# Kernel optimization log

Hardware: AMD Instinct MI355X
Metric: run time of the kernel (lower is better)

## Reference

```python
import jax, jax.numpy as jnp
import numpy as np

S, T, B, E, H, V = 64, 64, 64, 256, 256, 32000
PAD = 0


def _lstm_layer(X, Wih, Whh, b, h0, c0):
    # X: (time, B, in), torch gate order i,f,g,o
    def step(carry, x_t):
        h, c = carry
        z = x_t @ Wih.T + h @ Whh.T + b
        i, f, g, o = jnp.split(z, 4, axis=-1)
        c = jax.nn.sigmoid(f) * c + jax.nn.sigmoid(i) * jnp.tanh(g)
        h = jax.nn.sigmoid(o) * jnp.tanh(c)
        return (h, c), h
    (hT, cT), outs = jax.lax.scan(step, (h0, c0), X)
    return outs, hT, cT


def setup_inputs() -> dict:
    key = jax.random.key(0)
    ks = jax.random.split(key, 20)
    p = lambda k, shape: (jax.random.normal(k, shape, jnp.float32) * 0.05)
    inp = {
        "source_padded": jax.random.randint(ks[0], (S, B), 0, V, jnp.int32),
        "target_padded": jax.random.randint(ks[1], (T, B), 0, V, jnp.int32),
        "src_emb": p(ks[2], (V, E)),
        "tgt_emb": p(ks[3], (V, E)),
        "enc_Wih_f": p(ks[4], (4 * H, E)),
        "enc_Whh_f": p(ks[5], (4 * H, H)),
        "enc_b_f": p(ks[6], (4 * H,)),
        "enc_Wih_b": p(ks[7], (4 * H, E)),
        "enc_Whh_b": p(ks[8], (4 * H, H)),
        "enc_b_b": p(ks[9], (4 * H,)),
        "dec_Wih": p(ks[10], (4 * H, E + H)),
        "dec_Whh": p(ks[11], (4 * H, H)),
        "dec_b": p(ks[12], (4 * H,)),
        "Wh": p(ks[13], (H, 2 * H)),
        "Wc": p(ks[14], (H, 2 * H)),
        "Watt": p(ks[15], (H, 2 * H)),
        "Wcomb": p(ks[16], (H, 3 * H)),
        "Wvocab": p(ks[17], (V, H)),
    }
    return inp


def reference(source_padded, target_padded, src_emb, tgt_emb,
              enc_Wih_f, enc_Whh_f, enc_b_f, enc_Wih_b, enc_Whh_b, enc_b_b,
              dec_Wih, dec_Whh, dec_b, Wh, Wc, Watt, Wcomb, Wvocab):
    X = src_emb[source_padded]                      # (S,B,E)
    h0 = jnp.zeros((B, H), X.dtype)
    c0 = jnp.zeros((B, H), X.dtype)
    # bidirectional encoder (all sequences full length -> pack is identity)
    fwd_out, hf, cf = _lstm_layer(X, enc_Wih_f, enc_Whh_f, enc_b_f, h0, c0)
    bwd_out, hb, cb = _lstm_layer(X[::-1], enc_Wih_b, enc_Whh_b, enc_b_b, h0, c0)
    bwd_out = bwd_out[::-1]
    enc_hiddens = jnp.concatenate([fwd_out, bwd_out], -1).transpose(1, 0, 2)  # (B,S,2H)
    dec_h = jnp.concatenate([hf, hb], -1) @ Wh.T     # h_projection
    dec_c = jnp.concatenate([cf, cb], -1) @ Wc.T     # c_projection
    enc_proj = enc_hiddens @ Watt.T                  # (B,S,H)

    Y = tgt_emb[target_padded[:-1]]                  # (T-1,B,E)

    def dstep(carry, Y_t):
        h, c, o_prev = carry
        x = jnp.concatenate([Y_t, o_prev], -1)       # (B,E+H)
        z = x @ dec_Wih.T + h @ dec_Whh.T + dec_b
        i, f, g, o = jnp.split(z, 4, axis=-1)
        c = jax.nn.sigmoid(f) * c + jax.nn.sigmoid(i) * jnp.tanh(g)
        h = jax.nn.sigmoid(o) * jnp.tanh(c)
        e_t = jnp.einsum('bsh,bh->bs', enc_proj, h)  # attention scores
        alpha = jax.nn.softmax(e_t, axis=-1)         # no pads -> mask is no-op
        a_t = jnp.einsum('bs,bsd->bd', alpha, enc_hiddens)  # context (B,2H)
        O_t = jnp.tanh(jnp.concatenate([a_t, h], -1) @ Wcomb.T)  # dropout=eval
        return (h, c, O_t), O_t

    _, outs = jax.lax.scan(dstep, (dec_h, dec_c, jnp.zeros((B, H), X.dtype)), Y)
    P = jax.nn.log_softmax(outs @ Wvocab.T, axis=-1)          # (T-1,B,V)
    gold = jnp.take_along_axis(P, target_padded[1:][..., None], axis=-1)[..., 0]
    tmask = (target_padded[1:] != PAD).astype(P.dtype)
    return (gold * tmask).sum(axis=0)                          # (B,)
```

## Files before the change

kernel.cpp:

```cpp
#include <hip/hip_runtime.h>
#include <hip/hip_bf16.h>

static constexpr int S = 64, T = 64, B = 64, E = 256, H = 256, V = 32000;
static constexpr int H4 = 4 * H;
static constexpr int NCHUNK = 500;
static constexpr int NROW = (T - 1) * B;
static constexpr int LDP = 264;

typedef short bf16x8 __attribute__((ext_vector_type(8)));
typedef float f32x4 __attribute__((ext_vector_type(4)));
typedef unsigned long long ull;

__device__ __forceinline__ float sigf(float x) { return 1.0f / (1.0f + __expf(-x)); }
__device__ __forceinline__ float tanhfast(float x) { return 1.0f - 2.0f / (__expf(2.0f * x) + 1.0f); }
__device__ __forceinline__ float bflo(uint w) { return __uint_as_float(w << 16); }
__device__ __forceinline__ float bfhi(uint w) { return __uint_as_float(w & 0xffff0000u); }
__device__ __forceinline__ ushort f2bu(float x) {
  return __bfloat16_as_ushort(__float2bfloat16(x));
}

__device__ __forceinline__ void st_u32(uint* p, uint v) {
  __hip_atomic_store(p, v, __ATOMIC_RELAXED, __HIP_MEMORY_SCOPE_AGENT);
}
__device__ __forceinline__ uint ld_u32(const uint* p) {
  return __hip_atomic_load(p, __ATOMIC_RELAXED, __HIP_MEMORY_SCOPE_AGENT);
}
__device__ __forceinline__ void st_u64(ull* p, ull v) {
  __hip_atomic_store(p, v, __ATOMIC_RELAXED, __HIP_MEMORY_SCOPE_AGENT);
}
__device__ __forceinline__ ull ld_u64(const ull* p) {
  return __hip_atomic_load(p, __ATOMIC_RELAXED, __HIP_MEMORY_SCOPE_AGENT);
}
__device__ __forceinline__ ull pack2f(float a, float b) {
  return ((ull)__float_as_uint(b) << 32) | (ull)__float_as_uint(a);
}

__global__ __launch_bounds__(256) void k_cvt_bf16(const float* __restrict__ src,
                                                  __hip_bfloat16* __restrict__ dst, int n) {
  int i = blockIdx.x * 256 + threadIdx.x;
  if (i < n) dst[i] = __float2bfloat16(src[i]);
}

__global__ __launch_bounds__(256) void k_cvt_slice(const float* __restrict__ src,
                                                   __hip_bfloat16* __restrict__ dst) {
  int n = blockIdx.x, tid = threadIdx.x;
  dst[n * 256 + tid] = __float2bfloat16(src[n * 512 + tid]);
}

__global__ __launch_bounds__(256) void k_gather(const int* __restrict__ idx,
                                                const float* __restrict__ emb,
                                                __hip_bfloat16* __restrict__ dst) {
  int r = blockIdx.x, tid = threadIdx.x;
  dst[r * 256 + tid] = __float2bfloat16(emb[idx[r] * E + tid]);
}

__global__ __launch_bounds__(256) void k_pack4(const float* __restrict__ src,
                                               uint2* __restrict__ dst,
                                               int total, int jshift, int ld, int off) {
  int idx = blockIdx.x * 256 + threadIdx.x;
  if (idx >= total) return;
  int J = 1 << jshift;
  int i = idx >> jshift, j = idx & (J - 1);
  const float* s = src + (size_t)j * ld + off + 4 * i;
  float4 v = *(const float4*)s;
  uint2 o;
  o.x = (uint)f2bu(v.x) | ((uint)f2bu(v.y) << 16);
  o.y = (uint)f2bu(v.z) | ((uint)f2bu(v.w) << 16);
  dst[(size_t)i * J + j] = o;
}

__global__ __launch_bounds__(256) void k_xdec_init(const float* __restrict__ dech0,
                                                   __hip_bfloat16* __restrict__ Xd) {
  int b = blockIdx.x, tid = threadIdx.x;
  Xd[b * 512 + tid] = __float2bfloat16(dech0[b * 256 + tid]);
  Xd[b * 512 + 256 + tid] = __float2bfloat16(0.f);
}

#define MFMA_TILE_BODY(Abase, Wbase, rb, cb)                                     \
  const int tid = threadIdx.x;                                                   \
  const int lane = tid & 63, wid = tid >> 6;                                     \
  const int wr = wid >> 1, wc = wid & 1;                                         \
  const int l15 = lane & 15, l4 = lane >> 4;                                     \
  for (int it = 0; it < 8; it++) {                                               \
    int c = it * 256 + tid;                                                      \
    int row = c >> 5, off = (c & 31) * 8;                                        \
    *(uint4*)&Asl[row * LDP + off] =                                             \
        *(const uint4*)((Abase) + (size_t)((rb) + row) * 256 + off);             \
    *(uint4*)&Bsl[row * LDP + off] =                                             \
        *(const uint4*)((Wbase) + (size_t)((cb) + row) * 256 + off);             \
  }                                                                              \
  __syncthreads();                                                               \
  f32x4 acc[2][2];                                                               \
  for (int m = 0; m < 2; m++)                                                    \
    for (int n = 0; n < 2; n++) acc[m][n] = (f32x4){0.f, 0.f, 0.f, 0.f};         \
  for (int kk = 0; kk < 8; kk++) {                                               \
    int ko = kk * 32 + l4 * 8;                                                   \
    bf16x8 a0 = *(const bf16x8*)&Asl[(wr * 32 + l15) * LDP + ko];                \
    bf16x8 a1 = *(const bf16x8*)&Asl[(wr * 32 + 16 + l15) * LDP + ko];           \
    bf16x8 b0 = *(const bf16x8*)&Bsl[(wc * 32 + l15) * LDP + ko];                \
    bf16x8 b1 = *(const bf16x8*)&Bsl[(wc * 32 + 16 + l15) * LDP + ko];           \
    acc[0][0] = __builtin_amdgcn_mfma_f32_16x16x32_bf16(a0, b0, acc[0][0], 0, 0, 0); \
    acc[0][1] = __builtin_amdgcn_mfma_f32_16x16x32_bf16(a0, b1, acc[0][1], 0, 0, 0); \
    acc[1][0] = __builtin_amdgcn_mfma_f32_16x16x32_bf16(a1, b0, acc[1][0], 0, 0, 0); \
    acc[1][1] = __builtin_amdgcn_mfma_f32_16x16x32_bf16(a1, b1, acc[1][1], 0, 0, 0); \
  }

__global__ __launch_bounds__(256) void k_gemm_bias(
    const __hip_bfloat16* __restrict__ A, const __hip_bfloat16* __restrict__ W,
    const float* __restrict__ bias, float* __restrict__ C, int ldc) {
  __shared__ __align__(16) ushort Asl[64 * LDP];
  __shared__ __align__(16) ushort Bsl[64 * LDP];
  const int cb = blockIdx.x * 64, rb = blockIdx.y * 64;
  MFMA_TILE_BODY((const ushort*)A, (const ushort*)W, rb, cb)
  #pragma unroll
  for (int m = 0; m < 2; m++)
    #pragma unroll
    for (int n = 0; n < 2; n++) {
      int col = cb + wc * 32 + n * 16 + l15;
      float bv = bias[col];
      #pragma unroll
      for (int r = 0; r < 4; r++) {
        int row = rb + wr * 32 + m * 16 + l4 * 4 + r;
        C[(size_t)row * ldc + col] = acc[m][n][r] + bv;
      }
    }
}

__global__ __launch_bounds__(256) void k_encproj_mfma(
    const __hip_bfloat16* __restrict__ fwd_bf, const __hip_bfloat16* __restrict__ bwd_bf,
    const __hip_bfloat16* __restrict__ Watt_bf, __hip_bfloat16* __restrict__ encproj_bf) {
  __shared__ __align__(16) ushort Asl[64 * LDP];
  __shared__ __align__(16) ushort Bsl[64 * LDP];
  const int cb = blockIdx.x * 64, rb = blockIdx.y * 64;
  const int tid = threadIdx.x;
  const int lane = tid & 63, wid = tid >> 6;
  const int wr = wid >> 1, wc = wid & 1;
  const int l15 = lane & 15, l4 = lane >> 4;
  f32x4 acc[2][2];
  #pragma unroll
  for (int m = 0; m < 2; m++)
    #pragma unroll
    for (int n = 0; n < 2; n++) acc[m][n] = (f32x4){0.f, 0.f, 0.f, 0.f};
  for (int kt = 0; kt < 2; kt++) {
    if (kt) __syncthreads();
    for (int it = 0; it < 8; it++) {
      int c = it * 256 + tid;
      int row = c >> 5, off = (c & 31) * 8;
      int r = rb + row, s = r >> 6, bb = r & 63;
      const ushort* arow = (kt == 0)
          ? (const ushort*)fwd_bf + (size_t)(s * 64 + bb) * 256
          : (const ushort*)bwd_bf + (size_t)(s * 64 + bb) * 256;
      *(uint4*)&Asl[row * LDP + off] = *(const uint4*)(arow + off);
      *(uint4*)&Bsl[row * LDP + off] =
          *(const uint4*)((const ushort*)Watt_bf + (size_t)(cb + row) * 512 + kt * 256 + off);
    }
    __syncthreads();
    for (int kk = 0; kk < 8; kk++) {
      int ko = kk * 32 + l4 * 8;
      bf16x8 a0 = *(const bf16x8*)&Asl[(wr * 32 + l15) * LDP + ko];
      bf16x8 a1 = *(const bf16x8*)&Asl[(wr * 32 + 16 + l15) * LDP + ko];
      bf16x8 b0 = *(const bf16x8*)&Bsl[(wc * 32 + l15) * LDP + ko];
      bf16x8 b1 = *(const bf16x8*)&Bsl[(wc * 32 + 16 + l15) * LDP + ko];
      acc[0][0] = __builtin_amdgcn_mfma_f32_16x16x32_bf16(a0, b0, acc[0][0], 0, 0, 0);
      acc[0][1] = __builtin_amdgcn_mfma_f32_16x16x32_bf16(a0, b1, acc[0][1], 0, 0, 0);
      acc[1][0] = __builtin_amdgcn_mfma_f32_16x16x32_bf16(a1, b0, acc[1][0], 0, 0, 0);
      acc[1][1] = __builtin_amdgcn_mfma_f32_16x16x32_bf16(a1, b1, acc[1][1], 0, 0, 0);
    }
  }
  #pragma unroll
  for (int m = 0; m < 2; m++)
    #pragma unroll
    for (int n = 0; n < 2; n++) {
      int col = cb + wc * 32 + n * 16 + l15;
      #pragma unroll
      for (int r = 0; r < 4; r++) {
        int row = rb + wr * 32 + m * 16 + l4 * 4 + r;
        int s = row >> 6, bb = row & 63;
        ((ushort*)encproj_bf)[(size_t)(bb * 64 + s) * 256 + col] = f2bu(acc[m][n][r]);
      }
    }
}

__global__ __launch_bounds__(256) void k_vocab2(
    const __hip_bfloat16* __restrict__ outs_bf, const __hip_bfloat16* __restrict__ Wv,
    const int* __restrict__ tgt, float* __restrict__ part_max,
    float* __restrict__ part_sum, float* __restrict__ gold) {
  __shared__ __align__(16) ushort Asl[64 * LDP];
  __shared__ __align__(16) ushort Bsl[64 * LDP];
  __shared__ int goldcol[64];
  __shared__ float pm[64][2], ps[64][2];
  const int vb = blockIdx.x;
  const int tid = threadIdx.x;
  const int lane = tid & 63, wid = tid >> 6;
  const int wr = wid >> 1, wc = wid & 1;
  const int l15 = lane & 15, l4 = lane >> 4;
  for (int it = 0; it < 8; it++) {
    int c = it * 256 + tid;
    int row = c >> 5, off = (c & 31) * 8;
    *(uint4*)&Bsl[row * LDP + off] =
        *(const uint4*)((const ushort*)Wv + (size_t)(vb * 64 + row) * 256 + off);
  }
  for (int t = 0; t < T - 1; t++) {
    __syncthreads();
    for (int it = 0; it < 8; it++) {
      int c = it * 256 + tid;
      int row = c >> 5, off = (c & 31) * 8;
      *(uint4*)&Asl[row * LDP + off] =
          *(const uint4*)((const ushort*)outs_bf + (size_t)(t * 64 + row) * 256 + off);
    }
    if (tid < 64) goldcol[tid] = tgt[(t + 1) * B + tid];
    __syncthreads();
    f32x4 acc[2][2];
    #pragma unroll
    for (int m = 0; m < 2; m++)
      #pragma unroll
      for (int n = 0; n < 2; n++) acc[m][n] = (f32x4){0.f, 0.f, 0.f, 0.f};
    for (int kk = 0; kk < 8; kk++) {
      int ko = kk * 32 + l4 * 8;
      bf16x8 a0 = *(const bf16x8*)&Asl[(wr * 32 + l15) * LDP + ko];
      bf16x8 a1 = *(const bf16x8*)&Asl[(wr * 32 + 16 + l15) * LDP + ko];
      bf16x8 b0 = *(const bf16x8*)&Bsl[(wc * 32 + l15) * LDP + ko];
      bf16x8 b1 = *(const bf16x8*)&Bsl[(wc * 32 + 16 + l15) * LDP + ko];
      acc[0][0] = __builtin_amdgcn_mfma_f32_16x16x32_bf16(a0, b0, acc[0][0], 0, 0, 0);
      acc[0][1] = __builtin_amdgcn_mfma_f32_16x16x32_bf16(a0, b1, acc[0][1], 0, 0, 0);
      acc[1][0] = __builtin_amdgcn_mfma_f32_16x16x32_bf16(a1, b0, acc[1][0], 0, 0, 0);
      acc[1][1] = __builtin_amdgcn_mfma_f32_16x16x32_bf16(a1, b1, acc[1][1], 0, 0, 0);
    }
    #pragma unroll
    for (int m = 0; m < 2; m++) {
      #pragma unroll
      for (int r = 0; r < 4; r++) {
        int row_local = wr * 32 + m * 16 + l4 * 4 + r;
        int gc = goldcol[row_local];
        #pragma unroll
        for (int n = 0; n < 2; n++) {
          int col = vb * 64 + wc * 32 + n * 16 + l15;
          if (col == gc) gold[t * 64 + row_local] = acc[m][n][r];
        }
        float v = fmaxf(acc[m][0][r], acc[m][1][r]);
        #pragma unroll
        for (int o = 1; o < 16; o <<= 1) v = fmaxf(v, __shfl_xor(v, o));
        float e = __expf(acc[m][0][r] - v) + __expf(acc[m][1][r] - v);
        #pragma unroll
        for (int o = 1; o < 16; o <<= 1) e += __shfl_xor(e, o);
        if (l15 == 0) { pm[row_local][wc] = v; ps[row_local][wc] = e; }
      }
    }
    __syncthreads();
    if (tid < 64) {
      float m0 = pm[tid][0], m1 = pm[tid][1];
      float M = fmaxf(m0, m1);
      float Ss = ps[tid][0] * __expf(m0 - M) + ps[tid][1] * __expf(m1 - M);
      part_max[(size_t)vb * NROW + t * 64 + tid] = M;
      part_sum[(size_t)vb * NROW + t * 64 + tid] = Ss;
    }
  }
}

__global__ __launch_bounds__(256) void k_enc4(
    const float* __restrict__ XwF, const float* __restrict__ XwB,
    const float* __restrict__ WhhF, const float* __restrict__ WhhB,
    uint* __restrict__ Xenc_u32,
    __hip_bfloat16* __restrict__ fwd_bf, __hip_bfloat16* __restrict__ bwd_bf,
    float* __restrict__ Cfin, uint* __restrict__ eflags) {
  __shared__ __align__(16) ushort Wl[128 * 264];
  __shared__ __align__(16) ushort Xa[16 * 264];
  __shared__ float zz[4][8][33];
  __shared__ float hsb[8][32];
  const int id = blockIdx.x;
  const int g = id & 7, kb = id >> 3;
  const int dir = kb >> 3, s = kb & 7;
  const int tid = threadIdx.x;
  const float* Whh = dir ? WhhB : WhhF;
  const float* Xw = dir ? XwB : XwF;
  uint* fl = eflags + (size_t)(g * 2 + dir) * 8 * 32;
  for (int i = tid; i < 128 * 256; i += 256) {
    int c = i >> 8, k2 = i & 255;
    int gate = c >> 5, jj = c & 31;
    Wl[c * 264 + k2] = f2bu(Whh[(size_t)(gate * 256 + s * 32 + jj) * 256 + k2]);
  }
  for (int i = tid; i < 16 * 264; i += 256) Xa[i] = 0;
  const int lane = tid & 63, w = tid >> 6;
  const int l15 = lane & 15, l4 = lane >> 4;
  const int tb = tid >> 5, tjj = tid & 31;
  float c_reg = 0.f;
  __syncthreads();
  for (int st = 0; st < 64; st++) {
    const int ts = dir ? 63 - st : st;
    const int par = st & 1;
    const uint* Xr = Xenc_u32 + (size_t)(par * 2 + dir) * 8192;
    uint* Xo = Xenc_u32 + (size_t)((par ^ 1) * 2 + dir) * 8192;
    for (int i = tid; i < 8 * 128; i += 256) {
      int row = i >> 7, colu = i & 127;
      uint v = ld_u32(Xr + (size_t)(8 * g + row) * 128 + colu);
      *(uint*)&Xa[row * 264 + colu * 2] = v;
    }
    __syncthreads();
    f32x4 a0v = (f32x4){0.f, 0.f, 0.f, 0.f}, a1v = (f32x4){0.f, 0.f, 0.f, 0.f};
    for (int kk = 0; kk < 8; kk++) {
      bf16x8 af = *(const bf16x8*)&Xa[l15 * 264 + kk * 32 + l4 * 8];
      bf16x8 b0 = *(const bf16x8*)&Wl[((2 * w) * 16 + l15) * 264 + kk * 32 + l4 * 8];
      bf16x8 b1 = *(const bf16x8*)&Wl[((2 * w + 1) * 16 + l15) * 264 + kk * 32 + l4 * 8];
      a0v = __builtin_amdgcn_mfma_f32_16x16x32_bf16(af, b0, a0v, 0, 0, 0);
      a1v = __builtin_amdgcn_mfma_f32_16x16x32_bf16(af, b1, a1v, 0, 0, 0);
    }
    if (l4 < 2) {
      #pragma unroll
      for (int r = 0; r < 4; r++) {
        int b = l4 * 4 + r;
        zz[w][b][l15] = a0v[r];
        zz[w][b][16 + l15] = a1v[r];
      }
    }
    __syncthreads();
    {
      int gb = 8 * g + tb, j = 32 * s + tjj;
      const float* xw = Xw + (size_t)(ts * 64 + gb) * 1024;
      float zi = zz[0][tb][tjj] + xw[j];
      float zf = zz[1][tb][tjj] + xw[256 + j];
      float zg = zz[2][tb][tjj] + xw[512 + j];
      float zo = zz[3][tb][tjj] + xw[768 + j];
      float c = sigf(zf) * c_reg + sigf(zi) * tanhfast(zg);
      c_reg = c;
      float h = sigf(zo) * tanhfast(c);
      hsb[tb][tjj] = h;
      ushort hb = f2bu(h);
      if (dir == 0) ((ushort*)fwd_bf)[(size_t)(st * 64 + gb) * 256 + j] = hb;
      else          ((ushort*)bwd_bf)[(size_t)((63 - st) * 64 + gb) * 256 + j] = hb;
    }
    __syncthreads();
    if (tid < 128) {
      int tb2 = tid >> 4, p = tid & 15;
      uint v = (uint)f2bu(hsb[tb2][2 * p]) | ((uint)f2bu(hsb[tb2][2 * p + 1]) << 16);
      st_u32(Xo + (size_t)(8 * g + tb2) * 128 + 16 * s + p, v);
    }
    __syncthreads();
    if (tid == 0) st_u32(&fl[s * 32], (uint)(st + 1));
    if (tid < 8)
      while (ld_u32(&fl[tid * 32]) < (uint)(st + 1)) __builtin_amdgcn_s_sleep(2);
    asm volatile("" ::: "memory");
    __syncthreads();
  }
  Cfin[(size_t)(dir * 64 + 8 * g + tb) * 256 + 32 * s + tjj] = c_reg;
}

__global__ __launch_bounds__(256) void k_dec_init2(
    const __hip_bfloat16* __restrict__ Xenc, const float* __restrict__ Cfin,
    const float* __restrict__ Wh, const float* __restrict__ Wc,
    float* __restrict__ dech0, float* __restrict__ decc0) {
  int b = blockIdx.x, tid = threadIdx.x;
  __shared__ __align__(16) float ch[512], cc[512];
  ch[tid]       = __bfloat162float(Xenc[(size_t)(0 * 64 + b) * 256 + tid]);
  ch[256 + tid] = __bfloat162float(Xenc[(size_t)(1 * 64 + b) * 256 + tid]);
  cc[tid]       = Cfin[(size_t)(0 * 64 + b) * 256 + tid];
  cc[256 + tid] = Cfin[(size_t)(1 * 64 + b) * 256 + tid];
  __syncthreads();
  const float* wh = Wh + tid * 512;
  const float* wc = Wc + tid * 512;
  float ah = 0, ac = 0;
  for (int k = 0; k < 512; k += 4) {
    float4 hv = *(const float4*)&ch[k];
    float4 cv = *(const float4*)&cc[k];
    float4 w1 = *(const float4*)&wh[k];
    float4 w2 = *(const float4*)&wc[k];
    ah += hv.x * w1.x + hv.y * w1.y + hv.z * w1.z + hv.w * w1.w;
    ac += cv.x * w2.x + cv.y * w2.y + cv.z * w2.z + cv.w * w2.w;
  }
  dech0[b * 256 + tid] = ah;
  decc0[b * 256 + tid] = ac;
}

__global__ __launch_bounds__(512) void k_dec4(
    const float* __restrict__ YW, const float* __restrict__ dWih,
    const float* __restrict__ dWhh, const uint2* __restrict__ Wcq,
    const __hip_bfloat16* __restrict__ encproj_bf,
    const __hip_bfloat16* __restrict__ fwd_bf, const __hip_bfloat16* __restrict__ bwd_bf,
    const float* __restrict__ decc0, uint* __restrict__ Xd_u32,
    ull* __restrict__ zbuf_u64, __hip_bfloat16* __restrict__ outs_bf,
    uint* __restrict__ zflags, uint* __restrict__ aflags) {
  __shared__ __align__(16) char smem[153856];
  const int id = blockIdx.x;
  const int g = id & 7, kb = id >> 3;
  const int tid = threadIdx.x;
  uint* zfl = zflags + (size_t)g * 8 * 32;
  uint* afl = aflags + (size_t)g * 16 * 32;

  if (kb < 8) {
    const int s = kb;
    ushort* Wl = (ushort*)smem;
    ushort* Xa = (ushort*)(smem + 133120);
    float* zslds = (float*)(smem + 149760);
    for (int i = tid; i < 128 * 512; i += 512) {
      int c = i >> 9, k2 = i & 511;
      int gr = 128 * s + c;
      float v = (k2 < 256) ? dWhh[(size_t)gr * 256 + k2]
                           : dWih[(size_t)gr * 512 + 256 + (k2 - 256)];
      Wl[c * 520 + k2] = f2bu(v);
    }
    for (int i = tid; i < 16 * 520; i += 512) Xa[i] = 0;
    const int lane = tid & 63, w = tid >> 6;
    const int l15 = lane & 15, l4 = lane >> 4;
    __syncthreads();
    for (int t = 0; t < 63; t++) {
      if (t > 0) {
        if (tid < 16)
          while (ld_u32(&afl[tid * 32]) < (uint)t) __builtin_amdgcn_s_sleep(2);
        asm volatile("" ::: "memory");
        __syncthreads();
      }
      const uint* Xr = Xd_u32 + (size_t)(t & 1) * 16384;
      for (int i = tid; i < 8 * 256; i += 512) {
        int row = i >> 8, colu = i & 255;
        uint v = ld_u32(Xr + (size_t)(8 * g + row) * 256 + colu);
        *(uint*)&Xa[row * 520 + colu * 2] = v;
      }
      __syncthreads();
      f32x4 accv = (f32x4){0.f, 0.f, 0.f, 0.f};
      for (int kk = 0; kk < 16; kk++) {
        bf16x8 af = *(const bf16x8*)&Xa[l15 * 520 + kk * 32 + l4 * 8];
        bf16x8 bf = *(const bf16x8*)&Wl[(w * 16 + l15) * 520 + kk * 32 + l4 * 8];
        accv = __builtin_amdgcn_mfma_f32_16x16x32_bf16(af, bf, accv, 0, 0, 0);
      }
      if (l4 < 2) {
        #pragma unroll
        for (int r = 0; r < 4; r++) {
          int b = l4 * 4 + r;
          zslds[b * 128 + w * 16 + l15] = accv[r];
        }
      }
      __syncthreads();
      {
        int b = tid >> 6, cp = tid & 63;
        ull v = pack2f(zslds[b * 128 + 2 * cp], zslds[b * 128 + 2 * cp + 1]);
        st_u64(zbuf_u64 + (size_t)(8 * g + b) * 512 + 64 * s + cp, v);
      }
      __syncthreads();
      if (tid == 0) st_u32(&zfl[s * 32], (uint)(t + 1));
    }
  } else {
    const int lb = (kb - 8) >> 1, jh = (kb - 8) & 1;
    const int b = 8 * g + lb;
    ushort* ep = (ushort*)smem;
    ushort* eh = (ushort*)(smem + 33792);
    float* hn = (float*)(smem + 100352);
    float* xcomb = (float*)(smem + 101376);
    float* e_l = (float*)(smem + 104448);
    float* alpha_l = (float*)(smem + 104704);
    float* op_l = (float*)(smem + 104960);
    float* zstage = (float*)(smem + 107008);
    float* Ost = (float*)(smem + 111104);
    for (int i = tid; i < 64 * 256; i += 512) {
      int s2 = i >> 8, k2 = i & 255;
      ep[s2 * 264 + k2] = ((const ushort*)encproj_bf)[(size_t)(b * 64 + s2) * 256 + k2];
    }
    for (int i = tid; i < 64 * 512; i += 512) {
      int s2 = i >> 9, d = i & 511;
      ushort v = (d < 256) ? ((const ushort*)fwd_bf)[(size_t)(s2 * 64 + b) * 256 + d]
                           : ((const ushort*)bwd_bf)[(size_t)(s2 * 64 + b) * 256 + d - 256];
      eh[s2 * 520 + d] = v;
    }
    float c_reg = (tid < 256) ? decc0[(size_t)b * 256 + tid] : 0.f;
    __syncthreads();
    for (int t = 0; t < 63; t++) {
      if (tid < 8)
        while (ld_u32(&zfl[tid * 32]) < (uint)(t + 1)) __builtin_amdgcn_s_sleep(2);
      asm volatile("" ::: "memory");
      __syncthreads();
      {
        ull v = ld_u64(zbuf_u64 + (size_t)b * 512 + tid);
        ((ull*)zstage)[tid] = v;
      }
      __syncthreads();
      if (tid < 256) {
        const float* yw = YW + (size_t)(t * 64 + b) * 1024;
        float zi = zstage[tid] + yw[tid];
        float zf = zstage[256 + tid] + yw[256 + tid];
        float zg = zstage[512 + tid] + yw[512 + tid];
        float zo = zstage[768 + tid] + yw[768 + tid];
        float c = sigf(zf) * c_reg + sigf(zi) * tanhfast(zg);
        c_reg = c;
        hn[tid] = sigf(zo) * tanhfast(c);
      }
      __syncthreads();
      if (jh == 0 && tid < 128) {
        uint v = (uint)f2bu(hn[2 * tid]) | ((uint)f2bu(hn[2 * tid + 1]) << 16);
        st_u32(Xd_u32 + (size_t)((t & 1) ^ 1) * 16384 + (size_t)b * 256 + tid, v);
      }
      {
        int s2 = tid >> 3, q8 = tid & 7;
        const ushort* pr = ep + s2 * 264 + q8 * 32;
        const float* hq = hn + q8 * 32;
        float a = 0.f;
        #pragma unroll 8
        for (int kk = 0; kk < 32; kk += 2) {
          uint wv = *(const uint*)(pr + kk);
          a += bflo(wv) * hq[kk] + bfhi(wv) * hq[kk + 1];
        }
        a += __shfl_xor(a, 1);
        a += __shfl_xor(a, 2);
        a += __shfl_xor(a, 4);
        if (q8 == 0) e_l[s2] = a;
      }
      __syncthreads();
      if (tid < 64) {
        float e = e_l[tid];
        float mx = e;
        #pragma unroll
        for (int o = 32; o > 0; o >>= 1) mx = fmaxf(mx, __shfl_xor(mx, o));
        float p = __expf(e - mx);
        float ss = p;
        #pragma unroll
        for (int o = 32; o > 0; o >>= 1) ss += __shfl_xor(ss, o);
        alpha_l[tid] = p / ss;
      }
      __syncthreads();
      {
        float a = 0.f;
        const ushort* col = eh + tid;
        #pragma unroll 8
        for (int s2 = 0; s2 < 64; s2++)
          a += alpha_l[s2] * __uint_as_float(((uint)col[s2 * 520]) << 16);
        xcomb[tid] = a;
        if (tid < 256) xcomb[512 + tid] = hn[tid];
      }
      __syncthreads();
      {
        int jl = tid & 127, kq = tid >> 7;
        int j = jh * 128 + jl;
        const uint2* wp = Wcq + (size_t)(kq * 48) * 256 + j;
        const float4* x4 = (const float4*)xcomb + kq * 48;
        float a = 0.f;
        #pragma unroll 6
        for (int ii = 0; ii < 48; ii++) {
          uint2 wv = wp[(size_t)ii * 256];
          float4 xv = x4[ii];
          a += bflo(wv.x) * xv.x + bfhi(wv.x) * xv.y + bflo(wv.y) * xv.z + bfhi(wv.y) * xv.w;
        }
        op_l[kq * 128 + jl] = a;
      }
      __syncthreads();
      if (tid < 128) {
        float sum = op_l[tid] + op_l[128 + tid] + op_l[256 + tid] + op_l[384 + tid];
        float O = tanhfast(sum);
        Ost[tid] = O;
        ((ushort*)outs_bf)[(size_t)(t * 64 + b) * 256 + jh * 128 + tid] = f2bu(O);
      }
      __syncthreads();
      if (tid < 64) {
        uint v = (uint)f2bu(Ost[2 * tid]) | ((uint)f2bu(Ost[2 * tid + 1]) << 16);
        st_u32(Xd_u32 + (size_t)((t & 1) ^ 1) * 16384 + (size_t)b * 256 + 128 + jh * 64 + tid, v);
      }
      __syncthreads();
      if (tid == 0) st_u32(&afl[(lb * 2 + jh) * 32], (uint)(t + 1));
    }
  }
}

__global__ __launch_bounds__(256) void k_final(
    const float* __restrict__ part_max, const float* __restrict__ part_sum,
    const float* __restrict__ gold, const int* __restrict__ tgt,
    float* __restrict__ out) {
  int b = blockIdx.x, tid = threadIdx.x;
  int tq = tid >> 2, q = tid & 3;
  __shared__ float lm[64][4], ls[64][4];
  __shared__ float red[64];
  if (tq < T - 1) {
    int n = tq * B + b;
    float m = -__builtin_inff(), s = 0;
    for (int i = q; i < NCHUNK; i += 4) {
      float pmv = part_max[(size_t)i * NROW + n];
      float psv = part_sum[(size_t)i * NROW + n];
      float M2 = fmaxf(m, pmv);
      s = s * __expf(m - M2) + psv * __expf(pmv - M2);
      m = M2;
    }
    lm[tq][q] = m;
    ls[tq][q] = s;
  }
  __syncthreads();
  if (tid < T - 1) {
    float M = fmaxf(fmaxf(lm[tid][0], lm[tid][1]), fmaxf(lm[tid][2], lm[tid][3]));
    float Ss = ls[tid][0] * __expf(lm[tid][0] - M) + ls[tid][1] * __expf(lm[tid][1] - M) +
               ls[tid][2] * __expf(lm[tid][2] - M) + ls[tid][3] * __expf(lm[tid][3] - M);
    float lse = M + logf(Ss);
    int g = tgt[(tid + 1) * B + b];
    red[tid] = (g != 0) ? (gold[tid * B + b] - lse) : 0.f;
  }
  if (tid == T - 1) red[T - 1] = 0.f;
  __syncthreads();
  if (tid == 0) {
    float s = 0;
    for (int i = 0; i < T - 1; i++) s += red[i];
    out[b] = s;
  }
}

extern "C" void kernel_launch(void* const* d_in, const int* in_sizes, int n_in,
                              void* d_out, int out_size, void* d_ws, size_t ws_size,
                              hipStream_t stream) {
  (void)in_sizes; (void)n_in; (void)out_size; (void)ws_size;
  const int*   src   = (const int*)  d_in[0];
  const int*   tgt   = (const int*)  d_in[1];
  const float* semb  = (const float*)d_in[2];
  const float* temb  = (const float*)d_in[3];
  const float* WihF  = (const float*)d_in[4];
  const float* WhhF  = (const float*)d_in[5];
  const float* bF    = (const float*)d_in[6];
  const float* WihB  = (const float*)d_in[7];
  const float* WhhB  = (const float*)d_in[8];
  const float* bB    = (const float*)d_in[9];
  const float* dWih  = (const float*)d_in[10];
  const float* dWhh  = (const float*)d_in[11];
  const float* db    = (const float*)d_in[12];
  const float* Wh    = (const float*)d_in[13];
  const float* Wc    = (const float*)d_in[14];
  const float* Watt  = (const float*)d_in[15];
  const float* Wcomb = (const float*)d_in[16];
  const float* Wv    = (const float*)d_in[17];
  float* out = (float*)d_out;

  char* wp = (char*)d_ws;
  auto alloc = [&](size_t bytes) -> char* {
    char* p = wp;
    wp += (bytes + 255) & ~(size_t)255;
    return p;
  };
  float* XwF  = (float*)alloc((size_t)S * B * H4 * 4);
  float* XwB  = (float*)alloc((size_t)S * B * H4 * 4);
  float* YW   = (float*)alloc((size_t)(T - 1) * B * H4 * 4);
  __hip_bfloat16* fwd_bf     = (__hip_bfloat16*)alloc((size_t)S * B * H * 2);
  __hip_bfloat16* bwd_bf     = (__hip_bfloat16*)alloc((size_t)S * B * H * 2);
  __hip_bfloat16* encproj_bf = (__hip_bfloat16*)alloc((size_t)B * S * H * 2);
  __hip_bfloat16* Ag         = (__hip_bfloat16*)alloc((size_t)S * B * E * 2);
  __hip_bfloat16* Yg         = (__hip_bfloat16*)alloc((size_t)(T - 1) * B * E * 2);
  __hip_bfloat16* WihF_bf    = (__hip_bfloat16*)alloc((size_t)H4 * E * 2);
  __hip_bfloat16* WihB_bf    = (__hip_bfloat16*)alloc((size_t)H4 * E * 2);
  __hip_bfloat16* dWih_bf    = (__hip_bfloat16*)alloc((size_t)H4 * E * 2);
  __hip_bfloat16* Wv_bf      = (__hip_bfloat16*)alloc((size_t)V * H * 2);
  __hip_bfloat16* Watt_bf    = (__hip_bfloat16*)alloc((size_t)H * 512 * 2);
  __hip_bfloat16* outs_bf    = (__hip_bfloat16*)alloc((size_t)NROW * H * 2);
  uint2* Wcq = (uint2*)alloc((size_t)192 * 256 * 8);
  float* part_max = (float*)alloc((size_t)NCHUNK * NROW * 4);
  float* part_sum = (float*)alloc((size_t)NCHUNK * NROW * 4);
  float* gold     = (float*)alloc((size_t)NROW * 4);
  float* Cfin  = (float*)alloc((size_t)2 * B * H * 4);
  float* dech0 = (float*)alloc((size_t)B * H * 4);
  float* decc0 = (float*)alloc((size_t)B * H * 4);
  ull* zbuf_u64 = (ull*)alloc((size_t)B * 512 * 8);
  __hip_bfloat16* Xenc = (__hip_bfloat16*)alloc((size_t)2 * 2 * B * H * 2);
  __hip_bfloat16* Xdec = (__hip_bfloat16*)alloc((size_t)2 * B * 512 * 2);
  char* stateBase = wp;
  uint* eflags = (uint*)alloc(16 * 8 * 32 * 4);
  uint* zflags = (uint*)alloc(8 * 8 * 32 * 4);
  uint* aflags = (uint*)alloc(8 * 16 * 32 * 4);
  size_t stateBytes = (size_t)(wp - stateBase);
  hipMemsetAsync(stateBase, 0, stateBytes, stream);
  hipMemsetAsync(Xenc, 0, (size_t)2 * 2 * B * H * 2, stream);

  hipLaunchKernelGGL(k_cvt_bf16, dim3((H4 * E + 255) / 256), dim3(256), 0, stream,
                     WihF, WihF_bf, H4 * E);
  hipLaunchKernelGGL(k_cvt_bf16, dim3((H4 * E + 255) / 256), dim3(256), 0, stream,
                     WihB, WihB_bf, H4 * E);
  hipLaunchKernelGGL(k_cvt_slice, dim3(H4), dim3(256), 0, stream, dWih, dWih_bf);
  hipLaunchKernelGGL(k_cvt_bf16, dim3((V * H + 255) / 256), dim3(256), 0, stream,
                     Wv, Wv_bf, V * H);
  hipLaunchKernelGGL(k_cvt_bf16, dim3((H * 512 + 255) / 256), dim3(256), 0, stream,
                     Watt, Watt_bf, H * 512);
  hipLaunchKernelGGL(k_gather, dim3(S * B), dim3(256), 0, stream, src, semb, Ag);
  hipLaunchKernelGGL(k_gather, dim3((T - 1) * B), dim3(256), 0, stream, tgt, temb, Yg);
  hipLaunchKernelGGL(k_pack4, dim3(192 * 256 / 256), dim3(256), 0, stream,
                     Wcomb, Wcq, 192 * 256, 8, 768, 0);

  hipLaunchKernelGGL(k_gemm_bias, dim3(H4 / 64, S * B / 64), dim3(256), 0, stream,
                     Ag, WihF_bf, bF, XwF, H4);
  hipLaunchKernelGGL(k_gemm_bias, dim3(H4 / 64, S * B / 64), dim3(256), 0, stream,
                     Ag, WihB_bf, bB, XwB, H4);
  hipLaunchKernelGGL(k_gemm_bias, dim3(H4 / 64, (T - 1) * B / 64), dim3(256), 0, stream,
                     Yg, dWih_bf, db, YW, H4);

  hipLaunchKernelGGL(k_enc4, dim3(128), dim3(256), 0, stream,
                     XwF, XwB, WhhF, WhhB, (uint*)Xenc, fwd_bf, bwd_bf, Cfin, eflags);
  hipLaunchKernelGGL(k_dec_init2, dim3(B), dim3(256), 0, stream,
                     Xenc, Cfin, Wh, Wc, dech0, decc0);
  hipLaunchKernelGGL(k_xdec_init, dim3(B), dim3(256), 0, stream, dech0, Xdec);
  hipLaunchKernelGGL(k_encproj_mfma, dim3(4, 64), dim3(256), 0, stream,
                     fwd_bf, bwd_bf, Watt_bf, encproj_bf);

  hipLaunchKernelGGL(k_dec4, dim3(192), dim3(512), 0, stream,
                     YW, dWih, dWhh, Wcq, encproj_bf, fwd_bf, bwd_bf,
                     decc0, (uint*)Xdec, zbuf_u64, outs_bf, zflags, aflags);

  hipLaunchKernelGGL(k_vocab2, dim3(NCHUNK), dim3(256), 0, stream,
                     outs_bf, Wv_bf, tgt, part_max, part_sum, gold);
  hipLaunchKernelGGL(k_final, dim3(B), dim3(256), 0, stream,
                     part_max, part_sum, gold, tgt, out);
}
```

Baseline: 1.251 ms.

## Move decoder LSTM cell update into gate-GEMM blocks, drop z exchange buffer

The decoder gate-GEMM blocks now own complete i/f/g/o rows for their 32 hidden units. They apply the LSTM cell nonlinearity locally, keeping c in a register, and write bf16 h straight into the double-buffered Xdec. The attention blocks no longer read a fp32 z buffer or compute the cell; they just load h. This removes one global round trip of 64x1024 floats per step from the serial critical path. Separately, dec_init and xdec_init are fused into one kernel. In exchange, GEMM blocks must also wait on zflags from peer GEMM blocks to avoid overwriting Xdec early.

```diff
diff --git a/kernel.cpp b/kernel.cpp
--- a/kernel.cpp
+++ b/kernel.cpp
@@ -24,15 +24,6 @@
 }
 __device__ __forceinline__ uint ld_u32(const uint* p) {
   return __hip_atomic_load(p, __ATOMIC_RELAXED, __HIP_MEMORY_SCOPE_AGENT);
-}
-__device__ __forceinline__ void st_u64(ull* p, ull v) {
-  __hip_atomic_store(p, v, __ATOMIC_RELAXED, __HIP_MEMORY_SCOPE_AGENT);
-}
-__device__ __forceinline__ ull ld_u64(const ull* p) {
-  return __hip_atomic_load(p, __ATOMIC_RELAXED, __HIP_MEMORY_SCOPE_AGENT);
-}
-__device__ __forceinline__ ull pack2f(float a, float b) {
-  return ((ull)__float_as_uint(b) << 32) | (ull)__float_as_uint(a);
 }
 
 __global__ __launch_bounds__(256) void k_cvt_bf16(const float* __restrict__ src,
@@ -67,13 +58,6 @@
   o.x = (uint)f2bu(v.x) | ((uint)f2bu(v.y) << 16);
   o.y = (uint)f2bu(v.z) | ((uint)f2bu(v.w) << 16);
   dst[(size_t)i * J + j] = o;
-}
-
-__global__ __launch_bounds__(256) void k_xdec_init(const float* __restrict__ dech0,
-                                                   __hip_bfloat16* __restrict__ Xd) {
-  int b = blockIdx.x, tid = threadIdx.x;
-  Xd[b * 512 + tid] = __float2bfloat16(dech0[b * 256 + tid]);
-  Xd[b * 512 + 256 + tid] = __float2bfloat16(0.f);
 }
 
 #define MFMA_TILE_BODY(Abase, Wbase, rb, cb)                                     \
@@ -344,12 +328,13 @@
   Cfin[(size_t)(dir * 64 + 8 * g + tb) * 256 + 32 * s + tjj] = c_reg;
 }
 
-__global__ __launch_bounds__(256) void k_dec_init2(
+__global__ __launch_bounds__(256) void k_dec_init3(
     const __hip_bfloat16* __restrict__ Xenc, const float* __restrict__ Cfin,
     const float* __restrict__ Wh, const float* __restrict__ Wc,
-    float* __restrict__ dech0, float* __restrict__ decc0) {
+    uint* __restrict__ Xd_u32, float* __restrict__ decc0) {
   int b = blockIdx.x, tid = threadIdx.x;
   __shared__ __align__(16) float ch[512], cc[512];
+  __shared__ float hh[256];
   ch[tid]       = __bfloat162float(Xenc[(size_t)(0 * 64 + b) * 256 + tid]);
   ch[256 + tid] = __bfloat162float(Xenc[(size_t)(1 * 64 + b) * 256 + tid]);
   cc[tid]       = Cfin[(size_t)(0 * 64 + b) * 256 + tid];
@@ -366,19 +351,25 @@
     ah += hv.x * w1.x + hv.y * w1.y + hv.z * w1.z + hv.w * w1.w;
     ac += cv.x * w2.x + cv.y * w2.y + cv.z * w2.z + cv.w * w2.w;
   }
-  dech0[b * 256 + tid] = ah;
   decc0[b * 256 + tid] = ac;
-}
-
-__global__ __launch_bounds__(512) void k_dec4(
+  hh[tid] = ah;
+  __syncthreads();
+  if (tid < 128) {
+    uint v = (uint)f2bu(hh[2 * tid]) | ((uint)f2bu(hh[2 * tid + 1]) << 16);
+    Xd_u32[(size_t)b * 256 + tid] = v;
+    Xd_u32[(size_t)b * 256 + 128 + tid] = 0u;
+  }
+}
+
+__global__ __launch_bounds__(512) void k_dec5(
     const float* __restrict__ YW, const float* __restrict__ dWih,
     const float* __restrict__ dWhh, const uint2* __restrict__ Wcq,
     const __hip_bfloat16* __restrict__ encproj_bf,
     const __hip_bfloat16* __restrict__ fwd_bf, const __hip_bfloat16* __restrict__ bwd_bf,
     const float* __restrict__ decc0, uint* __restrict__ Xd_u32,
-    ull* __restrict__ zbuf_u64, __hip_bfloat16* __restrict__ outs_bf,
+    __hip_bfloat16* __restrict__ outs_bf,
     uint* __restrict__ zflags, uint* __restrict__ aflags) {
-  __shared__ __align__(16) char smem[153856];
+  __shared__ __align__(16) char smem[155648];
   const int id = blockIdx.x;
   const int g = id & 7, kb = id >> 3;
   const int tid = threadIdx.x;
@@ -390,9 +381,11 @@
     ushort* Wl = (ushort*)smem;
     ushort* Xa = (ushort*)(smem + 133120);
     float* zslds = (float*)(smem + 149760);
+    float* hsb = (float*)(smem + 153856);
     for (int i = tid; i < 128 * 512; i += 512) {
       int c = i >> 9, k2 = i & 511;
-      int gr = 128 * s + c;
+      int gate = c >> 5, jj = c & 31;
+      int gr = gate * 256 + 32 * s + jj;
       float v = (k2 < 256) ? dWhh[(size_t)gr * 256 + k2]
                            : dWih[(size_t)gr * 512 + 256 + (k2 - 256)];
       Wl[c * 520 + k2] = f2bu(v);
@@ -400,11 +393,18 @@
     for (int i = tid; i < 16 * 520; i += 512) Xa[i] = 0;
     const int lane = tid & 63, w = tid >> 6;
     const int l15 = lane & 15, l4 = lane >> 4;
+    float c_reg = 0.f;
+    if (tid < 256) {
+      int b = tid >> 5, jj = tid & 31;
+      c_reg = decc0[(size_t)(8 * g + b) * 256 + 32 * s + jj];
+    }
     __syncthreads();
     for (int t = 0; t < 63; t++) {
       if (t > 0) {
-        if (tid < 16)
-          while (ld_u32(&afl[tid * 32]) < (uint)t) __builtin_amdgcn_s_sleep(2);
+        if (tid < 8)
+          while (ld_u32(&zfl[tid * 32]) < (uint)t) __builtin_amdgcn_s_sleep(2);
+        else if (tid >= 64 && tid < 80)
+          while (ld_u32(&afl[(tid - 64) * 32]) < (uint)t) __builtin_amdgcn_s_sleep(2);
         asm volatile("" ::: "memory");
         __syncthreads();
       }
@@ -429,10 +429,23 @@
         }
       }
       __syncthreads();
-      {
-        int b = tid >> 6, cp = tid & 63;
-        ull v = pack2f(zslds[b * 128 + 2 * cp], zslds[b * 128 + 2 * cp + 1]);
-        st_u64(zbuf_u64 + (size_t)(8 * g + b) * 512 + 64 * s + cp, v);
+      if (tid < 256) {
+        int b = tid >> 5, jj = tid & 31;
+        int gb = 8 * g + b;
+        const float* yw = YW + (size_t)(t * 64 + gb) * 1024 + 32 * s + jj;
+        float zi = zslds[b * 128 + jj] + yw[0];
+        float zf = zslds[b * 128 + 32 + jj] + yw[256];
+        float zg = zslds[b * 128 + 64 + jj] + yw[512];
+        float zo = zslds[b * 128 + 96 + jj] + yw[768];
+        float c = sigf(zf) * c_reg + sigf(zi) * tanhfast(zg);
+        c_reg = c;
+        hsb[b * 32 + jj] = sigf(zo) * tanhfast(c);
+      }
+      __syncthreads();
+      if (tid < 128) {
+        int b = tid >> 4, p = tid & 15;
+        uint v = (uint)f2bu(hsb[b * 32 + 2 * p]) | ((uint)f2bu(hsb[b * 32 + 2 * p + 1]) << 16);
+        st_u32(Xd_u32 + (size_t)((t & 1) ^ 1) * 16384 + (size_t)(8 * g + b) * 256 + 16 * s + p, v);
       }
       __syncthreads();
       if (tid == 0) st_u32(&zfl[s * 32], (uint)(t + 1));
@@ -447,8 +460,7 @@
     float* e_l = (float*)(smem + 104448);
     float* alpha_l = (float*)(smem + 104704);
     float* op_l = (float*)(smem + 104960);
-    float* zstage = (float*)(smem + 107008);
-    float* Ost = (float*)(smem + 111104);
+    float* Ost = (float*)(smem + 107008);
     for (int i = tid; i < 64 * 256; i += 512) {
       int s2 = i >> 8, k2 = i & 255;
       ep[s2 * 264 + k2] = ((const ushort*)encproj_bf)[(size_t)(b * 64 + s2) * 256 + k2];
@@ -459,33 +471,18 @@
                            : ((const ushort*)bwd_bf)[(size_t)(s2 * 64 + b) * 256 + d - 256];
       eh[s2 * 520 + d] = v;
     }
-    float c_reg = (tid < 256) ? decc0[(size_t)b * 256 + tid] : 0.f;
     __syncthreads();
     for (int t = 0; t < 63; t++) {
       if (tid < 8)
         while (ld_u32(&zfl[tid * 32]) < (uint)(t + 1)) __builtin_amdgcn_s_sleep(2);
       asm volatile("" ::: "memory");
       __syncthreads();
-      {
-        ull v = ld_u64(zbuf_u64 + (size_t)b * 512 + tid);
-        ((ull*)zstage)[tid] = v;
-      }
-      __syncthreads();
-      if (tid < 256) {
-        const float* yw = YW + (size_t)(t * 64 + b) * 1024;
-        float zi = zstage[tid] + yw[tid];
-        float zf = zstage[256 + tid] + yw[256 + tid];
-        float zg = zstage[512 + tid] + yw[512 + tid];
-        float zo = zstage[768 + tid] + yw[768 + tid];
-        float c = sigf(zf) * c_reg + sigf(zi) * tanhfast(zg);
-        c_reg = c;
-        hn[tid] = sigf(zo) * tanhfast(c);
-      }
-      __syncthreads();
-      if (jh == 0 && tid < 128) {
-        uint v = (uint)f2bu(hn[2 * tid]) | ((uint)f2bu(hn[2 * tid + 1]) << 16);
-        st_u32(Xd_u32 + (size_t)((t & 1) ^ 1) * 16384 + (size_t)b * 256 + tid, v);
-      }
+      if (tid < 128) {
+        uint v = ld_u32(Xd_u32 + (size_t)((t & 1) ^ 1) * 16384 + (size_t)b * 256 + tid);
+        hn[2 * tid] = bflo(v);
+        hn[2 * tid + 1] = bfhi(v);
+      }
+      __syncthreads();
       {
         int s2 = tid >> 3, q8 = tid & 7;
         const ushort* pr = ep + s2 * 264 + q8 * 32;
@@ -644,11 +641,9 @@
   float* part_sum = (float*)alloc((size_t)NCHUNK * NROW * 4);
   float* gold     = (float*)alloc((size_t)NROW * 4);
   float* Cfin  = (float*)alloc((size_t)2 * B * H * 4);
-  float* dech0 = (float*)alloc((size_t)B * H * 4);
   float* decc0 = (float*)alloc((size_t)B * H * 4);
-  ull* zbuf_u64 = (ull*)alloc((size_t)B * 512 * 8);
   __hip_bfloat16* Xenc = (__hip_bfloat16*)alloc((size_t)2 * 2 * B * H * 2);
-  __hip_bfloat16* Xdec = (__hip_bfloat16*)alloc((size_t)2 * B * 512 * 2);
+  uint* Xdec = (uint*)alloc((size_t)2 * B * 256 * 4);
   char* stateBase = wp;
   uint* eflags = (uint*)alloc(16 * 8 * 32 * 4);
   uint* zflags = (uint*)alloc(8 * 8 * 32 * 4);
@@ -680,15 +675,14 @@
 
   hipLaunchKernelGGL(k_enc4, dim3(128), dim3(256), 0, stream,
                      XwF, XwB, WhhF, WhhB, (uint*)Xenc, fwd_bf, bwd_bf, Cfin, eflags);
-  hipLaunchKernelGGL(k_dec_init2, dim3(B), dim3(256), 0, stream,
-                     Xenc, Cfin, Wh, Wc, dech0, decc0);
-  hipLaunchKernelGGL(k_xdec_init, dim3(B), dim3(256), 0, stream, dech0, Xdec);
+  hipLaunchKernelGGL(k_dec_init3, dim3(B), dim3(256), 0, stream,
+                     Xenc, Cfin, Wh, Wc, Xdec, decc0);
   hipLaunchKernelGGL(k_encproj_mfma, dim3(4, 64), dim3(256), 0, stream,
                      fwd_bf, bwd_bf, Watt_bf, encproj_bf);
 
-  hipLaunchKernelGGL(k_dec4, dim3(192), dim3(512), 0, stream,
+  hipLaunchKernelGGL(k_dec5, dim3(192), dim3(512), 0, stream,
                      YW, dWih, dWhh, Wcq, encproj_bf, fwd_bf, bwd_bf,
-                     decc0, (uint*)Xdec, zbuf_u64, outs_bf, zflags, aflags);
+                     decc0, Xdec, outs_bf, zflags, aflags);
 
   hipLaunchKernelGGL(k_vocab2, dim3(NCHUNK), dim3(256), 0, stream,
                      outs_bf, Wv_bf, tgt, part_max, part_sum, gold);
```

Result: no change. 1.253 ms (+0.2%).
